# Optimization experiments

Measured on AMD Instinct MI355X. Metric: run time of the kernel, lower is better.

## Reference

```python
import jax, jax.numpy as jnp
import numpy as np

K = 32          # init k
E = 0.003       # EMA rate e


def setup_inputs() -> dict:
    key = jax.random.key(0)
    k1, _ = jax.random.split(key)
    features = jax.random.normal(k1, (512, 6, 8192), dtype=jnp.float32)
    threshold = jnp.zeros((1,), dtype=jnp.float32)
    return {"features": features, "threshold": threshold}


def reference(features, threshold):
    batch_size, n_layers, d_features = features.shape
    batch_k = K * batch_size * n_layers
    flat = features.reshape(-1)                      # [B*L*D]
    topk_vals, topk_idxs = jax.lax.top_k(flat, batch_k)
    topk_vals = jax.nn.relu(topk_vals)
    out = jnp.zeros_like(flat).at[topk_idxs].set(topk_vals)
    out = out.reshape(batch_size, n_layers, d_features)
    min_k = jax.lax.stop_gradient(jnp.min(topk_vals))
    new_threshold = (1.0 - E) * threshold + E * min_k
    return out, new_threshold
```

## Files before the change

kernel.cpp:

```cpp
#include <hip/hip_runtime.h>
#include <stdint.h>

#define N_ELEMS   25165824
#define K_TOTAL   98304u
#define EMA_RATE  0.003f

#define NBINS1     16384
#define BIN1_SHIFT 18
#define NBINS2     4096
#define NBINS3     64
#define LCAP       2048
#define EQCAP      1024

__device__ __forceinline__ unsigned f2key(float x) {
    unsigned u = __float_as_uint(x);
    return (u & 0x80000000u) ? ~u : (u | 0x80000000u);
}
__device__ __forceinline__ float key2f(unsigned key) {
    unsigned u = (key & 0x80000000u) ? (key & 0x7FFFFFFFu) : ~key;
    return __uint_as_float(u);
}

__global__ __launch_bounds__(512) void hist1_kernel(
        const float4* __restrict__ in, unsigned* __restrict__ ghist, int nvec) {
    __shared__ unsigned h[NBINS1];
    for (int i = threadIdx.x; i < NBINS1; i += blockDim.x) h[i] = 0;
    __syncthreads();
    int stride = gridDim.x * blockDim.x;
    for (int i = blockIdx.x * blockDim.x + threadIdx.x; i < nvec; i += stride) {
        float4 v = in[i];
        atomicAdd(&h[f2key(v.x) >> BIN1_SHIFT], 1u);
        atomicAdd(&h[f2key(v.y) >> BIN1_SHIFT], 1u);
        atomicAdd(&h[f2key(v.z) >> BIN1_SHIFT], 1u);
        atomicAdd(&h[f2key(v.w) >> BIN1_SHIFT], 1u);
    }
    __syncthreads();
    for (int i = threadIdx.x; i < NBINS1; i += blockDim.x) {
        unsigned c = h[i];
        if (c) atomicAdd(&ghist[i], c);
    }
}

__global__ __launch_bounds__(512) void find_bin_kernel(
        const unsigned* __restrict__ ghist, unsigned* __restrict__ res) {
    __shared__ unsigned psum[512];
    const int T = 512;
    const int GB = NBINS1 / T;
    int t = threadIdx.x;
    int hi = NBINS1 - 1 - t * GB;
    unsigned s = 0;
    for (int j = 0; j < GB; ++j) s += ghist[hi - j];
    psum[t] = s;
    __syncthreads();
    for (int off = 1; off < T; off <<= 1) {
        unsigned o = (t >= off) ? psum[t - off] : 0u;
        __syncthreads();
        psum[t] += o;
        __syncthreads();
    }
    unsigned cum = psum[t] - s;
    for (int j = 0; j < GB; ++j) {
        unsigned c = ghist[hi - j];
        if (cum < K_TOTAL && cum + c >= K_TOTAL) {
            res[0] = (unsigned)(hi - j);
            res[1] = cum;
        }
        cum += c;
    }
}

__device__ __forceinline__ float proc_elem(
        float x, unsigned idx, unsigned b,
        float* lval, unsigned* lidx, unsigned* lcnt,
        float* cval, unsigned* cidx, unsigned* gcnt, unsigned cap) {
    unsigned bin = f2key(x) >> BIN1_SHIFT;
    if (bin < b) return 0.0f;
    if (bin > b) return fmaxf(x, 0.0f);
    unsigned p = atomicAdd(lcnt, 1u);
    if (p < LCAP) { lval[p] = x; lidx[p] = idx; }
    else {
        unsigned g = atomicAdd(gcnt, 1u);
        if (g < cap) { cval[g] = x; cidx[g] = idx; }
    }
    return 0.0f;
}

__global__ __launch_bounds__(256) void pass2_kernel(
        const float4* __restrict__ in, float4* __restrict__ out,
        const unsigned* __restrict__ res,
        float* __restrict__ cval, unsigned* __restrict__ cidx,
        unsigned* __restrict__ gcnt, unsigned cap, int nvec) {
    __shared__ float    lval[LCAP];
    __shared__ unsigned lidx[LCAP];
    __shared__ unsigned lcnt;
    __shared__ unsigned base;
    if (threadIdx.x == 0) lcnt = 0;
    __syncthreads();
    unsigned b = res[0];
    int stride = gridDim.x * blockDim.x;
    for (int i = blockIdx.x * blockDim.x + threadIdx.x; i < nvec; i += stride) {
        float4 v = in[i];
        unsigned idx = 4u * (unsigned)i;
        float4 o;
        o.x = proc_elem(v.x, idx + 0u, b, lval, lidx, &lcnt, cval, cidx, gcnt, cap);
        o.y = proc_elem(v.y, idx + 1u, b, lval, lidx, &lcnt, cval, cidx, gcnt, cap);
        o.z = proc_elem(v.z, idx + 2u, b, lval, lidx, &lcnt, cval, cidx, gcnt, cap);
        o.w = proc_elem(v.w, idx + 3u, b, lval, lidx, &lcnt, cval, cidx, gcnt, cap);
        out[i] = o;
    }
    __syncthreads();
    unsigned n = min(lcnt, (unsigned)LCAP);
    if (threadIdx.x == 0) base = atomicAdd(gcnt, n);
    __syncthreads();
    for (unsigned j = threadIdx.x; j < n; j += blockDim.x) {
        unsigned p = base + j;
        if (p < cap) { cval[p] = lval[j]; cidx[p] = lidx[j]; }
    }
}

__global__ __launch_bounds__(1024) void pass3_kernel(
        const float* __restrict__ cval, const unsigned* __restrict__ cidx,
        const unsigned* __restrict__ gcnt, const unsigned* __restrict__ res,
        unsigned cap, float* __restrict__ out,
        const float* __restrict__ thr_in, float* __restrict__ thr_out) {
    __shared__ unsigned h2[NBINS2];
    __shared__ unsigned psum[1024];
    __shared__ unsigned h3[NBINS3];
    __shared__ unsigned eqidx[EQCAP];
    __shared__ unsigned eqcnt;
    __shared__ unsigned sh_b2, sh_need2, sh_b3, sh_need3;

    int t = threadIdx.x;
    unsigned nc   = min(*gcnt, cap);
    unsigned b    = res[0];
    unsigned need = K_TOTAL - res[1];

    for (int i = t; i < NBINS2; i += 1024) h2[i] = 0;
    if (t == 0) eqcnt = 0;
    __syncthreads();

    for (unsigned i = t; i < nc; i += 1024) {
        unsigned key = f2key(cval[i]);
        atomicAdd(&h2[(key >> 6) & (NBINS2 - 1)], 1u);
    }
    __syncthreads();

    const int GB = NBINS2 / 1024;
    int hi = NBINS2 - 1 - t * GB;
    unsigned s = 0;
    for (int j = 0; j < GB; ++j) s += h2[hi - j];
    psum[t] = s;
    __syncthreads();
    for (int off = 1; off < 1024; off <<= 1) {
        unsigned o = (t >= off) ? psum[t - off] : 0u;
        __syncthreads();
        psum[t] += o;
        __syncthreads();
    }
    unsigned cum = psum[t] - s;
    for (int j = 0; j < GB; ++j) {
        unsigned c = h2[hi - j];
        if (cum < need && cum + c >= need) {
            sh_b2 = (unsigned)(hi - j);
            sh_need2 = need - cum;
        }
        cum += c;
    }
    __syncthreads();
    unsigned b2 = sh_b2, need2 = sh_need2;

    for (int i = t; i < NBINS3; i += 1024) h3[i] = 0;
    __syncthreads();
    for (unsigned i = t; i < nc; i += 1024) {
        unsigned key = f2key(cval[i]);
        if (((key >> 6) & (NBINS2 - 1)) == b2) atomicAdd(&h3[key & 63u], 1u);
    }
    __syncthreads();
    if (t < NBINS3) {
        int bin = NBINS3 - 1 - t;
        unsigned cum3 = 0;
        for (int j = bin + 1; j < NBINS3; ++j) cum3 += h3[j];
        unsigned c = h3[bin];
        if (cum3 < need2 && cum3 + c >= need2) {
            sh_b3 = (unsigned)bin;
            sh_need3 = need2 - cum3;
        }
    }
    __syncthreads();
    unsigned keyv  = (b << BIN1_SHIFT) | (b2 << 6) | sh_b3;
    unsigned need3 = sh_need3;

    for (unsigned i = t; i < nc; i += 1024) {
        float x = cval[i];
        unsigned key = f2key(x);
        if (key > keyv) {
            out[cidx[i]] = fmaxf(x, 0.0f);
        } else if (key == keyv) {
            unsigned p = atomicAdd(&eqcnt, 1u);
            if (p < EQCAP) eqidx[p] = cidx[i];
        }
    }
    __syncthreads();

    unsigned ne = min(eqcnt, (unsigned)EQCAP);
    float vv = key2f(keyv);
    for (unsigned e = t; e < ne; e += 1024) {
        unsigned my = eqidx[e];
        unsigned rank = 0;
        for (unsigned f = 0; f < ne; ++f) rank += (eqidx[f] < my) ? 1u : 0u;
        if (rank < need3) out[my] = fmaxf(vv, 0.0f);
    }

    if (t == 0) {
        float mink = fmaxf(vv, 0.0f);
        thr_out[0] = (1.0f - EMA_RATE) * thr_in[0] + EMA_RATE * mink;
    }
}

extern "C" void kernel_launch(void* const* d_in, const int* in_sizes, int n_in,
                              void* d_out, int out_size, void* d_ws, size_t ws_size,
                              hipStream_t stream) {
    const float* feat   = (const float*)d_in[0];
    const float* thr_in = (const float*)d_in[1];
    float* out = (float*)d_out;
    int N    = in_sizes[0];
    int nvec = N / 4;

    uint8_t* w = (uint8_t*)d_ws;
    unsigned* ghist = (unsigned*)w;
    unsigned* res   = (unsigned*)(w + (64 << 10));
    unsigned* gcnt  = (unsigned*)(w + (64 << 10) + 64);
    size_t cand_off = (size_t)(128 << 10);
    size_t cap_sz   = (ws_size > cand_off) ? (ws_size - cand_off) / 8 : 0;
    unsigned cap    = (unsigned)(cap_sz < (size_t)(1 << 20) ? cap_sz : (size_t)(1 << 20));
    float*    cval  = (float*)(w + cand_off);
    unsigned* cidx  = (unsigned*)(w + cand_off + (size_t)cap * 4);

    hipMemsetAsync(d_ws, 0, (64 << 10) + 128, stream);

    hist1_kernel  <<<1024, 512, 0, stream>>>((const float4*)feat, ghist, nvec);
    find_bin_kernel<<<1,   512, 0, stream>>>(ghist, res);
    pass2_kernel  <<<2048, 256, 0, stream>>>((const float4*)feat, (float4*)out, res,
                                             cval, cidx, gcnt, cap, nvec);
    pass3_kernel  <<<1,   1024, 0, stream>>>(cval, cidx, gcnt, res, cap,
                                             out, thr_in, out + N);
}
```

Measured before the change: 258.6 us.

## Replace full histogram pass with sampled threshold estimate and single candidate pass

Instead of a full-data histogram pass followed by a second full read, the code builds a histogram from a small prefix sample to estimate a conservative lower-bound key. It then does one full pass that collects candidates above that bound and histograms them. A memset zeroes the output, and multi-stage refinement then scatters only the winners. This removes one full read of the input but adds a full-size memset write. It also relies on the sample bound being low enough: if the prefix is unrepresentative and fewer than k elements pass the bound, the result is wrong.

```diff
diff --git a/kernel.cpp b/kernel.cpp
--- a/kernel.cpp
+++ b/kernel.cpp
@@ -1,16 +1,18 @@
 #include <hip/hip_runtime.h>
 #include <stdint.h>
 
-#define N_ELEMS   25165824
 #define K_TOTAL   98304u
 #define EMA_RATE  0.003f
 
-#define NBINS1     16384
-#define BIN1_SHIFT 18
-#define NBINS2     4096
-#define NBINS3     64
-#define LCAP       2048
-#define EQCAP      1024
+#define SBINS      16384
+#define SBIN_SHIFT 18
+#define SAMPLE_VEC 131072
+#define STARGET    8192u
+#define P2_BINS    4096
+#define P2_SHIFT   12
+#define LCAP       1024
+#define CAP2       65536u
+#define EQCAP      256
 
 __device__ __forceinline__ unsigned f2key(float x) {
     unsigned u = __float_as_uint(x);
@@ -21,38 +23,113 @@
     return __uint_as_float(u);
 }
 
-__global__ __launch_bounds__(512) void hist1_kernel(
-        const float4* __restrict__ in, unsigned* __restrict__ ghist, int nvec) {
-    __shared__ unsigned h[NBINS1];
-    for (int i = threadIdx.x; i < NBINS1; i += blockDim.x) h[i] = 0;
-    __syncthreads();
-    int stride = gridDim.x * blockDim.x;
-    for (int i = blockIdx.x * blockDim.x + threadIdx.x; i < nvec; i += stride) {
+__global__ __launch_bounds__(256) void sample_hist_kernel(
+        const float4* __restrict__ in, unsigned* __restrict__ shist) {
+    __shared__ unsigned h[SBINS];
+    for (int i = threadIdx.x; i < SBINS; i += 256) h[i] = 0;
+    __syncthreads();
+    int stride = gridDim.x * 256;
+    for (int i = blockIdx.x * 256 + threadIdx.x; i < SAMPLE_VEC; i += stride) {
         float4 v = in[i];
-        atomicAdd(&h[f2key(v.x) >> BIN1_SHIFT], 1u);
-        atomicAdd(&h[f2key(v.y) >> BIN1_SHIFT], 1u);
-        atomicAdd(&h[f2key(v.z) >> BIN1_SHIFT], 1u);
-        atomicAdd(&h[f2key(v.w) >> BIN1_SHIFT], 1u);
-    }
-    __syncthreads();
-    for (int i = threadIdx.x; i < NBINS1; i += blockDim.x) {
+        atomicAdd(&h[f2key(v.x) >> SBIN_SHIFT], 1u);
+        atomicAdd(&h[f2key(v.y) >> SBIN_SHIFT], 1u);
+        atomicAdd(&h[f2key(v.z) >> SBIN_SHIFT], 1u);
+        atomicAdd(&h[f2key(v.w) >> SBIN_SHIFT], 1u);
+    }
+    __syncthreads();
+    for (int i = threadIdx.x; i < SBINS; i += 256) {
+        unsigned c = h[i];
+        if (c) atomicAdd(&shist[i], c);
+    }
+}
+
+__global__ __launch_bounds__(256) void sample_scan_kernel(
+        const unsigned* __restrict__ shist, unsigned* __restrict__ res) {
+    __shared__ unsigned psum[256];
+    const int GB = SBINS / 256;
+    int t = threadIdx.x;
+    int hi = SBINS - 1 - t * GB;
+    unsigned s = 0;
+    for (int j = 0; j < GB; ++j) s += shist[hi - j];
+    psum[t] = s;
+    __syncthreads();
+    for (int off = 1; off < 256; off <<= 1) {
+        unsigned o = (t >= off) ? psum[t - off] : 0u;
+        __syncthreads();
+        psum[t] += o;
+        __syncthreads();
+    }
+    unsigned cum = psum[t] - s;
+    for (int j = 0; j < GB; ++j) {
+        unsigned c = shist[hi - j];
+        if (cum < STARGET && cum + c >= STARGET) {
+            unsigned bin = (unsigned)(hi - j);
+            unsigned bb = (bin > 0) ? bin - 1 : 0;
+            res[0] = bb << SBIN_SHIFT;
+        }
+        cum += c;
+    }
+}
+
+__global__ __launch_bounds__(256) void main_pass_kernel(
+        const float4* __restrict__ in, const unsigned* __restrict__ res,
+        float* __restrict__ cval, unsigned* __restrict__ cidx,
+        unsigned* __restrict__ gcnt, unsigned* __restrict__ ghist,
+        unsigned cap, int nvec) {
+    __shared__ unsigned h[P2_BINS];
+    __shared__ float    lval[LCAP];
+    __shared__ unsigned lidx[LCAP];
+    __shared__ unsigned lcnt, lbase;
+    for (int i = threadIdx.x; i < P2_BINS; i += 256) h[i] = 0;
+    if (threadIdx.x == 0) lcnt = 0;
+    __syncthreads();
+    unsigned base = res[0];
+    int stride = gridDim.x * 256;
+    for (int i = blockIdx.x * 256 + threadIdx.x; i < nvec; i += stride) {
+        float4 v = in[i];
+        unsigned idx = 4u * (unsigned)i;
+        #pragma unroll
+        for (int c = 0; c < 4; ++c) {
+            float x = (c == 0) ? v.x : (c == 1) ? v.y : (c == 2) ? v.z : v.w;
+            unsigned key = f2key(x);
+            if (key >= base) {
+                unsigned g = (key - base) >> P2_SHIFT;
+                if (g > P2_BINS - 1) g = P2_BINS - 1;
+                atomicAdd(&h[g], 1u);
+                unsigned p = atomicAdd(&lcnt, 1u);
+                if (p < LCAP) { lval[p] = x; lidx[p] = idx + c; }
+                else {
+                    unsigned q = atomicAdd(gcnt, 1u);
+                    if (q < cap) { cval[q] = x; cidx[q] = idx + c; }
+                }
+            }
+        }
+    }
+    __syncthreads();
+    unsigned n = min(lcnt, (unsigned)LCAP);
+    if (threadIdx.x == 0) lbase = atomicAdd(gcnt, n);
+    __syncthreads();
+    for (unsigned j = threadIdx.x; j < n; j += 256) {
+        unsigned p = lbase + j;
+        if (p < cap) { cval[p] = lval[j]; cidx[p] = lidx[j]; }
+    }
+    for (int i = threadIdx.x; i < P2_BINS; i += 256) {
         unsigned c = h[i];
         if (c) atomicAdd(&ghist[i], c);
     }
 }
 
-__global__ __launch_bounds__(512) void find_bin_kernel(
-        const unsigned* __restrict__ ghist, unsigned* __restrict__ res) {
-    __shared__ unsigned psum[512];
-    const int T = 512;
-    const int GB = NBINS1 / T;
+__global__ __launch_bounds__(256) void find_g_kernel(
+        const unsigned* __restrict__ ghist, unsigned* __restrict__ res2) {
+    __shared__ unsigned psum[256];
+    const int GB = P2_BINS / 256;
     int t = threadIdx.x;
-    int hi = NBINS1 - 1 - t * GB;
+    int hi = P2_BINS - 1 - t * GB;
     unsigned s = 0;
     for (int j = 0; j < GB; ++j) s += ghist[hi - j];
     psum[t] = s;
     __syncthreads();
-    for (int off = 1; off < T; off <<= 1) {
+    for (int off = 1; off < 256; off <<= 1) {
         unsigned o = (t >= off) ? psum[t - off] : 0u;
         __syncthreads();
         psum[t] += o;
@@ -62,96 +139,72 @@
     for (int j = 0; j < GB; ++j) {
         unsigned c = ghist[hi - j];
         if (cum < K_TOTAL && cum + c >= K_TOTAL) {
-            res[0] = (unsigned)(hi - j);
-            res[1] = cum;
+            res2[0] = (unsigned)(hi - j);
+            res2[1] = K_TOTAL - cum;
         }
         cum += c;
     }
 }
 
-__device__ __forceinline__ float proc_elem(
-        float x, unsigned idx, unsigned b,
-        float* lval, unsigned* lidx, unsigned* lcnt,
-        float* cval, unsigned* cidx, unsigned* gcnt, unsigned cap) {
-    unsigned bin = f2key(x) >> BIN1_SHIFT;
-    if (bin < b) return 0.0f;
-    if (bin > b) return fmaxf(x, 0.0f);
-    unsigned p = atomicAdd(lcnt, 1u);
-    if (p < LCAP) { lval[p] = x; lidx[p] = idx; }
-    else {
-        unsigned g = atomicAdd(gcnt, 1u);
-        if (g < cap) { cval[g] = x; cidx[g] = idx; }
-    }
-    return 0.0f;
-}
-
-__global__ __launch_bounds__(256) void pass2_kernel(
-        const float4* __restrict__ in, float4* __restrict__ out,
-        const unsigned* __restrict__ res,
-        float* __restrict__ cval, unsigned* __restrict__ cidx,
-        unsigned* __restrict__ gcnt, unsigned cap, int nvec) {
-    __shared__ float    lval[LCAP];
-    __shared__ unsigned lidx[LCAP];
-    __shared__ unsigned lcnt;
-    __shared__ unsigned base;
-    if (threadIdx.x == 0) lcnt = 0;
-    __syncthreads();
-    unsigned b = res[0];
-    int stride = gridDim.x * blockDim.x;
-    for (int i = blockIdx.x * blockDim.x + threadIdx.x; i < nvec; i += stride) {
-        float4 v = in[i];
-        unsigned idx = 4u * (unsigned)i;
-        float4 o;
-        o.x = proc_elem(v.x, idx + 0u, b, lval, lidx, &lcnt, cval, cidx, gcnt, cap);
-        o.y = proc_elem(v.y, idx + 1u, b, lval, lidx, &lcnt, cval, cidx, gcnt, cap);
-        o.z = proc_elem(v.z, idx + 2u, b, lval, lidx, &lcnt, cval, cidx, gcnt, cap);
-        o.w = proc_elem(v.w, idx + 3u, b, lval, lidx, &lcnt, cval, cidx, gcnt, cap);
-        out[i] = o;
-    }
-    __syncthreads();
-    unsigned n = min(lcnt, (unsigned)LCAP);
-    if (threadIdx.x == 0) base = atomicAdd(gcnt, n);
-    __syncthreads();
-    for (unsigned j = threadIdx.x; j < n; j += blockDim.x) {
-        unsigned p = base + j;
-        if (p < cap) { cval[p] = lval[j]; cidx[p] = lidx[j]; }
-    }
-}
-
-__global__ __launch_bounds__(1024) void pass3_kernel(
+__global__ __launch_bounds__(256) void scatter_kernel(
         const float* __restrict__ cval, const unsigned* __restrict__ cidx,
         const unsigned* __restrict__ gcnt, const unsigned* __restrict__ res,
-        unsigned cap, float* __restrict__ out,
+        const unsigned* __restrict__ res2,
+        float* __restrict__ cval2, unsigned* __restrict__ cidx2,
+        unsigned* __restrict__ cnt2, unsigned cap,
+        float* __restrict__ out) {
+    unsigned nc = min(*gcnt, cap);
+    unsigned base = res[0];
+    unsigned gstar = res2[0];
+    int stride = gridDim.x * 256;
+    for (unsigned i = blockIdx.x * 256 + threadIdx.x; i < nc; i += stride) {
+        float x = cval[i];
+        unsigned key = f2key(x);
+        unsigned g = (key - base) >> P2_SHIFT;
+        if (g > P2_BINS - 1) g = P2_BINS - 1;
+        if (g > gstar) {
+            out[cidx[i]] = fmaxf(x, 0.0f);
+        } else if (g == gstar) {
+            unsigned p = atomicAdd(cnt2, 1u);
+            if (p < CAP2) { cval2[p] = x; cidx2[p] = cidx[i]; }
+        }
+    }
+}
+
+__global__ __launch_bounds__(256) void final_kernel(
+        const float* __restrict__ cval2, const unsigned* __restrict__ cidx2,
+        const unsigned* __restrict__ cnt2,
+        const unsigned* __restrict__ res, const unsigned* __restrict__ res2,
+        float* __restrict__ out,
         const float* __restrict__ thr_in, float* __restrict__ thr_out) {
-    __shared__ unsigned h2[NBINS2];
-    __shared__ unsigned psum[1024];
-    __shared__ unsigned h3[NBINS3];
+    __shared__ unsigned h[1 << P2_SHIFT];
+    __shared__ unsigned psum[256];
     __shared__ unsigned eqidx[EQCAP];
     __shared__ unsigned eqcnt;
-    __shared__ unsigned sh_b2, sh_need2, sh_b3, sh_need3;
-
+    __shared__ unsigned sh_low, sh_need3;
+    const int NB = 1 << P2_SHIFT;
     int t = threadIdx.x;
-    unsigned nc   = min(*gcnt, cap);
-    unsigned b    = res[0];
-    unsigned need = K_TOTAL - res[1];
-
-    for (int i = t; i < NBINS2; i += 1024) h2[i] = 0;
+    unsigned nc2   = min(*cnt2, CAP2);
+    unsigned base3 = res[0] + (res2[0] << P2_SHIFT);
+    unsigned need2 = res2[1];
+
+    for (int i = t; i < NB; i += 256) h[i] = 0;
     if (t == 0) eqcnt = 0;
     __syncthreads();
-
-    for (unsigned i = t; i < nc; i += 1024) {
-        unsigned key = f2key(cval[i]);
-        atomicAdd(&h2[(key >> 6) & (NBINS2 - 1)], 1u);
-    }
-    __syncthreads();
-
-    const int GB = NBINS2 / 1024;
-    int hi = NBINS2 - 1 - t * GB;
+    for (unsigned i = t; i < nc2; i += 256) {
+        unsigned low = f2key(cval2[i]) - base3;
+        if (low > (unsigned)(NB - 1)) low = NB - 1;
+        atomicAdd(&h[low], 1u);
+    }
+    __syncthreads();
+
+    const int GB = NB / 256;
+    int hi = NB - 1 - t * GB;
     unsigned s = 0;
-    for (int j = 0; j < GB; ++j) s += h2[hi - j];
+    for (int j = 0; j < GB; ++j) s += h[hi - j];
     psum[t] = s;
     __syncthreads();
-    for (int off = 1; off < 1024; off <<= 1) {
+    for (int off = 1; off < 256; off <<= 1) {
         unsigned o = (t >= off) ? psum[t - off] : 0u;
         __syncthreads();
         psum[t] += o;
@@ -159,52 +212,32 @@
     }
     unsigned cum = psum[t] - s;
     for (int j = 0; j < GB; ++j) {
-        unsigned c = h2[hi - j];
-        if (cum < need && cum + c >= need) {
-            sh_b2 = (unsigned)(hi - j);
-            sh_need2 = need - cum;
+        unsigned c = h[hi - j];
+        if (cum < need2 && cum + c >= need2) {
+            sh_low = (unsigned)(hi - j);
+            sh_need3 = need2 - cum;
         }
         cum += c;
     }
     __syncthreads();
-    unsigned b2 = sh_b2, need2 = sh_need2;
-
-    for (int i = t; i < NBINS3; i += 1024) h3[i] = 0;
-    __syncthreads();
-    for (unsigned i = t; i < nc; i += 1024) {
-        unsigned key = f2key(cval[i]);
-        if (((key >> 6) & (NBINS2 - 1)) == b2) atomicAdd(&h3[key & 63u], 1u);
-    }
-    __syncthreads();
-    if (t < NBINS3) {
-        int bin = NBINS3 - 1 - t;
-        unsigned cum3 = 0;
-        for (int j = bin + 1; j < NBINS3; ++j) cum3 += h3[j];
-        unsigned c = h3[bin];
-        if (cum3 < need2 && cum3 + c >= need2) {
-            sh_b3 = (unsigned)bin;
-            sh_need3 = need2 - cum3;
-        }
-    }
-    __syncthreads();
-    unsigned keyv  = (b << BIN1_SHIFT) | (b2 << 6) | sh_b3;
-    unsigned need3 = sh_need3;
-
-    for (unsigned i = t; i < nc; i += 1024) {
-        float x = cval[i];
+    unsigned kth_key = base3 + sh_low;
+    unsigned need3   = sh_need3;
+
+    for (unsigned i = t; i < nc2; i += 256) {
+        float x = cval2[i];
         unsigned key = f2key(x);
-        if (key > keyv) {
-            out[cidx[i]] = fmaxf(x, 0.0f);
-        } else if (key == keyv) {
+        if (key > kth_key) {
+            out[cidx2[i]] = fmaxf(x, 0.0f);
+        } else if (key == kth_key) {
             unsigned p = atomicAdd(&eqcnt, 1u);
-            if (p < EQCAP) eqidx[p] = cidx[i];
+            if (p < EQCAP) eqidx[p] = cidx2[i];
         }
     }
     __syncthreads();
 
     unsigned ne = min(eqcnt, (unsigned)EQCAP);
-    float vv = key2f(keyv);
-    for (unsigned e = t; e < ne; e += 1024) {
+    float vv = key2f(kth_key);
+    for (unsigned e = t; e < ne; e += 256) {
         unsigned my = eqidx[e];
         unsigned rank = 0;
         for (unsigned f = 0; f < ne; ++f) rank += (eqidx[f] < my) ? 1u : 0u;
@@ -227,21 +260,33 @@
     int nvec = N / 4;
 
     uint8_t* w = (uint8_t*)d_ws;
-    unsigned* ghist = (unsigned*)w;
-    unsigned* res   = (unsigned*)(w + (64 << 10));
-    unsigned* gcnt  = (unsigned*)(w + (64 << 10) + 64);
-    size_t cand_off = (size_t)(128 << 10);
-    size_t cap_sz   = (ws_size > cand_off) ? (ws_size - cand_off) / 8 : 0;
-    unsigned cap    = (unsigned)(cap_sz < (size_t)(1 << 20) ? cap_sz : (size_t)(1 << 20));
+    unsigned* shist = (unsigned*)w;
+    unsigned* ghist = (unsigned*)(w + (64 << 10));
+    unsigned* ctr   = (unsigned*)(w + (80 << 10));
+    unsigned* gcnt  = ctr + 0;
+    unsigned* cnt2  = ctr + 1;
+    unsigned* res   = ctr + 4;
+    unsigned* res2  = ctr + 8;
+
+    size_t cand_off = (size_t)1 << 20;
+    size_t avail    = (ws_size > cand_off + (CAP2 * 8 + 4096))
+                        ? (ws_size - cand_off - CAP2 * 8 - 4096) / 8 : 0;
+    unsigned cap = (unsigned)((avail < (size_t)(4u << 20)) ? avail : (size_t)(4u << 20));
     float*    cval  = (float*)(w + cand_off);
     unsigned* cidx  = (unsigned*)(w + cand_off + (size_t)cap * 4);
-
-    hipMemsetAsync(d_ws, 0, (64 << 10) + 128, stream);
-
-    hist1_kernel  <<<1024, 512, 0, stream>>>((const float4*)feat, ghist, nvec);
-    find_bin_kernel<<<1,   512, 0, stream>>>(ghist, res);
-    pass2_kernel  <<<2048, 256, 0, stream>>>((const float4*)feat, (float4*)out, res,
-                                             cval, cidx, gcnt, cap, nvec);
-    pass3_kernel  <<<1,   1024, 0, stream>>>(cval, cidx, gcnt, res, cap,
-                                             out, thr_in, out + N);
-}
+    float*    cval2 = (float*)(w + cand_off + (size_t)cap * 8);
+    unsigned* cidx2 = (unsigned*)(w + cand_off + (size_t)cap * 8 + CAP2 * 4);
+
+    hipMemsetAsync(d_ws, 0, (80 << 10) + 64, stream);
+    hipMemsetAsync(d_out, 0, (size_t)N * 4, stream);
+
+    sample_hist_kernel<<<128, 256, 0, stream>>>((const float4*)feat, shist);
+    sample_scan_kernel<<<1,   256, 0, stream>>>(shist, res);
+    main_pass_kernel  <<<1536, 256, 0, stream>>>((const float4*)feat, res,
+                                                 cval, cidx, gcnt, ghist, cap, nvec);
+    find_g_kernel     <<<1,   256, 0, stream>>>(ghist, res2);
+    scatter_kernel    <<<64,  256, 0, stream>>>(cval, cidx, gcnt, res, res2,
+                                                cval2, cidx2, cnt2, cap, out);
+    final_kernel      <<<1,   256, 0, stream>>>(cval2, cidx2, cnt2, res, res2,
+                                                out, thr_in, out + N);
+}
```

New measurement: 266.3 us. 3.0% more time.
